# Kernel tuning notes

Hardware: AMD Instinct MI355X
Metric: run time of the kernel (lower is better)

The kernel has to match this reference:

```python
import jax, jax.numpy as jnp
import numpy as np

NHEAD, DK, DV = 8, 32, 32
GRAPH = [[1,2,3,6,7],[1,2,4],[1,3,5],[2,4],[3,5],[1,6,8,12],[1,7,9,13],[6,8,10],[7,9,13],[8,10],[9,11],[9,12,14],[11,13,15],[12,14,16],[13,15,17],[14,16],[15,17]]
_idx = np.zeros((17,5), np.int32); _val = np.zeros((17,5), bool)
for _i, _nb in enumerate(GRAPH):
    for _j, _n in enumerate(_nb):
        _idx[_i,_j] = _n-1; _val[_i,_j] = True
NBR_IDX = jnp.asarray(_idx)            # (17,5) neighbor table (pad idx 0)
NBR_VALID = jnp.asarray(_val)          # (17,5) valid-neighbor mask
ATT_MASK = jnp.asarray(np.concatenate([_val, np.ones((17,2), bool)], 1))  # (17,7): 5 local + 2 global keys
INV_SQRT_DK = float(1.0/np.sqrt(DK))

def _ln_c(x, g, b, eps=1e-6):
    # LayerNorm over channel axis of (B,C,L)
    m = x.mean(1, keepdims=True)
    v = x.var(1, keepdims=True)
    return (x - m) * jax.lax.rsqrt(v + eps) * g[None,:,None] + b[None,:,None]

def _bn3(x, g, b, eps=1e-5):
    # BatchNorm1d (training batch stats) per channel over (B,L); x:(B,C,L)
    m = x.mean((0,2), keepdims=True)
    v = x.var((0,2), keepdims=True)
    return (x - m) * jax.lax.rsqrt(v + eps) * g[None,:,None] + b[None,:,None]

def _pos_ffn(x, w1, b1, w2, b2, g, b):
    # x:(B,C,L); Linear over C, relu, Linear back, residual, BatchNorm1d
    h = jax.nn.relu(jnp.einsum('bcl,hc->bhl', x, w1) + b1[None,:,None])
    y = jnp.einsum('bhl,ch->bcl', h, w2) + b2[None,:,None] + x
    return _bn3(y, g, b)

def _unfold(t):
    # t:(B,C,17) -> (B,C,5,17): per-node 5-wide neighbor window, zero padded
    g = t[:,:,NBR_IDX]                              # (B,C,17,5)
    g = jnp.where(NBR_VALID[None,None], g, 0.0)
    return jnp.transpose(g, (0,1,3,2))

def _sju(xn, ax, wq,bq,wk,bk,wv,bv, bng,bnb, f1w,f1b,f2w,f2b,fg,fb):
    B, C, L = xn.shape
    q = (jnp.einsum('oc,bcl->bol', wq, xn) + bq[None,:,None]).reshape(B,NHEAD,DK,L)
    kx = jnp.einsum('oc,bcl->bol', wk, xn) + bk[None,:,None]
    vx = jnp.einsum('oc,bcl->bol', wv, xn) + bv[None,:,None]
    k = _unfold(kx).reshape(B,NHEAD,DK,5,L)
    v = _unfold(vx).reshape(B,NHEAD,DV,5,L)
    ak = (jnp.einsum('oc,bcal->boal', wk, ax) + bk[None,:,None,None]).reshape(B,NHEAD,DK,2,L)
    av = (jnp.einsum('oc,bcal->boal', wv, ax) + bv[None,:,None,None]).reshape(B,NHEAD,DV,2,L)
    k = jnp.concatenate([k, ak], 3)                 # (B,H,dk,7,L)
    v = jnp.concatenate([v, av], 3)
    pre = jnp.einsum('bhdl,bhdwl->bhwl', q, k) * INV_SQRT_DK
    pre = jnp.where(ATT_MASK.T[None,None], pre, -jnp.inf)
    a = jax.nn.softmax(pre, axis=2)
    att = jnp.einsum('bhwl,bhdwl->bhdl', a, v).reshape(B,C,L)
    ret = _bn3(xn + att, bng, bnb)
    return _pos_ffn(ret, f1w,f1b,f2w,f2b,fg,fb)

def _sru(x, y, wq,bq,wk,bk,wv,bv, bng,bnb, f1w,f1b,f2w,f2b,fg,fb):
    # x:(B,C) relay, y:(B,C,Ly) keys/values
    B, C = x.shape
    q = (x @ wq.T + bq).reshape(B,NHEAD,DK)
    k = (jnp.einsum('oc,bcl->bol', wk, y) + bk[None,:,None]).reshape(B,NHEAD,DK,-1)
    v = (jnp.einsum('oc,bcl->bol', wv, y) + bv[None,:,None]).reshape(B,NHEAD,DV,-1)
    a = jax.nn.softmax(jnp.einsum('bhd,bhdl->bhl', q, k) * INV_SQRT_DK, axis=2)
    att = jnp.einsum('bhl,bhdl->bhd', a, v).reshape(B,C)
    ret = _bn3((x + att)[:,:,None], bng, bnb)
    return _pos_ffn(ret, f1w,f1b,f2w,f2b,fg,fb)[:,:,0]

def _forward(data, ln_g, ln_b, jq_w, jq_b, jk_w, jk_b, jv_w, jv_b, jbn_g, jbn_b, jf1_w, jf1_b, jf2_w, jf2_b, jfbn_g, jfbn_b, rq_w, rq_b, rk_w, rk_b, rv_w, rv_b, rbn_g, rbn_b, rf1_w, rf1_b, rf2_w, rf2_b, rfbn_g, rfbn_b):
    B, C, V, T = data.shape
    embs = jnp.transpose(data, (0,3,1,2)).reshape(B*T, C, V)   # fold time into batch
    nodes = embs
    relay = embs.mean(2)                                       # (BT,C)
    # ax: per node the 2 extra keys = its own original embedding + relay (fixed across layers)
    ax = jnp.stack([embs, jnp.broadcast_to(relay[:,:,None], embs.shape)], axis=2)  # (BT,C,2,V)
    for i in range(ln_g.shape[0]):
        xn = _ln_c(nodes, ln_g[i], ln_b[i])
        nodes = jax.nn.leaky_relu(_sju(xn, ax, jq_w[i],jq_b[i],jk_w[i],jk_b[i],jv_w[i],jv_b[i],jbn_g[i],jbn_b[i],jf1_w[i],jf1_b[i],jf2_w[i],jf2_b[i],jfbn_g[i],jfbn_b[i]), 0.01)
        y = jnp.concatenate([relay[:,:,None], nodes], axis=2)   # (BT,C,18)
        relay = jax.nn.leaky_relu(_sru(relay, y, rq_w[i],rq_b[i],rk_w[i],rk_b[i],rv_w[i],rv_b[i],rbn_g[i],rbn_b[i],rf1_w[i],rf1_b[i],rf2_w[i],rf2_b[i],rfbn_g[i],rfbn_b[i]), 0.01)
    return jnp.transpose(nodes.reshape(B,T,C,V), (0,2,3,1))

def setup_inputs():
    key = jax.random.key(0)
    Lyr, C, DIN, B, T, V = 2, 256, 1024, 4, 256, 17
    ks = jax.random.split(key, 40)
    ctr = [0]
    def nxt():
        k = ks[ctr[0]]; ctr[0] += 1; return k
    def w(shape, s=0.05):
        return jax.random.normal(nxt(), shape, jnp.float32) * s
    ones = lambda: jnp.ones((Lyr, C), jnp.float32)
    zeros = lambda: jnp.zeros((Lyr, C), jnp.float32)
    inp = {'data': jax.random.normal(nxt(), (B,C,V,T), jnp.float32),
           'ln_g': ones(), 'ln_b': zeros()}
    for p in ('j', 'r'):
        inp[p+'q_w'] = w((Lyr,C,C)); inp[p+'q_b'] = w((Lyr,C))
        inp[p+'k_w'] = w((Lyr,C,C)); inp[p+'k_b'] = w((Lyr,C))
        inp[p+'v_w'] = w((Lyr,C,C)); inp[p+'v_b'] = w((Lyr,C))
        inp[p+'bn_g'] = ones(); inp[p+'bn_b'] = zeros()
        inp[p+'f1_w'] = w((Lyr,DIN,C)); inp[p+'f1_b'] = w((Lyr,DIN))
        inp[p+'f2_w'] = w((Lyr,C,DIN)); inp[p+'f2_b'] = w((Lyr,C))
        inp[p+'fbn_g'] = ones(); inp[p+'fbn_b'] = zeros()
    return inp

def reference(data, ln_g, ln_b, jq_w, jq_b, jk_w, jk_b, jv_w, jv_b, jbn_g, jbn_b, jf1_w, jf1_b, jf2_w, jf2_b, jfbn_g, jfbn_b, rq_w, rq_b, rk_w, rk_b, rv_w, rv_b, rbn_g, rbn_b, rf1_w, rf1_b, rf2_w, rf2_b, rfbn_g, rfbn_b):
    return _forward(data, ln_g, ln_b, jq_w, jq_b, jk_w, jk_b, jv_w, jv_b, jbn_g, jbn_b, jf1_w, jf1_b, jf2_w, jf2_b, jfbn_g, jfbn_b, rq_w, rq_b, rk_w, rk_b, rv_w, rv_b, rbn_g, rbn_b, rf1_w, rf1_b, rf2_w, rf2_b, rfbn_g, rfbn_b)
```

## Files before the change

### kernel.cpp

```cpp
#include <hip/hip_runtime.h>
#include <hip/hip_bf16.h>


using bf16 = __hip_bfloat16;
typedef __attribute__((ext_vector_type(8))) short bf16x8v;
typedef __attribute__((ext_vector_type(4))) float f32x4;

namespace {
constexpr int kBT = 1024;
constexpr int kC = 256;
constexpr int kV = 17;
constexpr int kT = 256;
constexpr int kDIN = 1024;
constexpr int kRows = kBT * kV;
constexpr int kRowsE = kRows + kBT;
constexpr float kInvSqrtDk = 0.17677669529663687f;
constexpr size_t SZ_BIG = (size_t)kRows * kC;
}

__constant__ int c_nbi[17][5] = {
    {0, 1, 2, 5, 6},   {0, 1, 3, 0, 0},   {0, 2, 4, 0, 0},  {1, 3, 0, 0, 0},
    {2, 4, 0, 0, 0},   {0, 5, 7, 11, 0},  {0, 6, 8, 12, 0}, {5, 7, 9, 0, 0},
    {6, 8, 12, 0, 0},  {7, 9, 0, 0, 0},   {8, 10, 0, 0, 0}, {8, 11, 13, 0, 0},
    {10, 12, 14, 0, 0},{11, 13, 15, 0, 0},{12, 14, 16, 0, 0},
    {13, 15, 0, 0, 0}, {14, 16, 0, 0, 0}};
__constant__ int c_ncnt[17] = {5, 3, 3, 2, 2, 4, 4, 3, 3, 2, 2, 3, 3, 3, 3, 2, 2};

__device__ inline float bf2f(unsigned short s) {
  unsigned int u = ((unsigned int)s) << 16;
  float f;
  __builtin_memcpy(&f, &u, 4);
  return f;
}
__device__ inline unsigned short f2bf(float f) {
  unsigned int u;
  __builtin_memcpy(&u, &f, 4);
  unsigned int r = (u + 0x7fffu + ((u >> 16) & 1u)) >> 16;
  return (unsigned short)r;
}
__device__ inline float4 ldbf4(const bf16* p) {
  ushort4 u = *(const ushort4*)p;
  return make_float4(bf2f(u.x), bf2f(u.y), bf2f(u.z), bf2f(u.w));
}
__device__ inline void stbf4(bf16* p, float4 v) {
  ushort4 u = make_ushort4(f2bf(v.x), f2bf(v.y), f2bf(v.z), f2bf(v.w));
  *(ushort4*)p = u;
}
__device__ inline float dot4(float4 a, float4 b) {
  return a.x * b.x + a.y * b.y + a.z * b.z + a.w * b.w;
}

__device__ inline void async16(const bf16* g, bf16* l) {
  __builtin_amdgcn_global_load_lds(
      (const __attribute__((address_space(1))) void*)g,
      (__attribute__((address_space(3))) void*)l, 16, 0, 0);
}

template <int KT>
__global__ __launch_bounds__(256) void k_mfma_gemm(
    const bf16* __restrict__ A, const bf16* __restrict__ W,
    const float* __restrict__ bias, const float* __restrict__ res,
    float* __restrict__ outF, bf16* __restrict__ outB, int N, int flags) {
  __shared__ bf16 As[2][128 * 64];
  __shared__ bf16 Bs[2][128 * 64];
  const int tid = threadIdx.x;
  const int wave = tid >> 6;
  const int lane = tid & 63;
  const int row0 = blockIdx.x * 128;
  const int col0 = blockIdx.y * 128;

  const int sub = lane >> 2;
  const int kq = (lane & 3) * 8;
  const int rg0 = (2 * wave + 0) * 16;
  const int rg1 = (2 * wave + 1) * 16;
  const bf16* ag0 = A + (size_t)(row0 + rg0 + sub) * KT + kq;
  const bf16* ag1 = A + (size_t)(row0 + rg1 + sub) * KT + kq;
  const bf16* bg0 = W + (size_t)(col0 + rg0 + sub) * KT + kq;
  const bf16* bg1 = W + (size_t)(col0 + rg1 + sub) * KT + kq;

  const int wm = wave >> 1, wn = wave & 1;
  const int fr = lane & 15;
  const int fk = (lane >> 4) * 8;

  f32x4 acc[4][4];
#pragma unroll
  for (int i = 0; i < 4; ++i)
#pragma unroll
    for (int j = 0; j < 4; ++j) acc[i][j] = (f32x4){0.f, 0.f, 0.f, 0.f};

#define STAGE64(buf, koff)                                   \
  do {                                                       \
    _Pragma("unroll") for (int kc = 0; kc < 2; ++kc) {       \
      const int off = (koff) + kc * 32;                      \
      async16(ag0 + off, &As[(buf)][kc * 4096 + rg0 * 32]);  \
      async16(ag1 + off, &As[(buf)][kc * 4096 + rg1 * 32]);  \
      async16(bg0 + off, &Bs[(buf)][kc * 4096 + rg0 * 32]);  \
      async16(bg1 + off, &Bs[(buf)][kc * 4096 + rg1 * 32]);  \
    }                                                        \
  } while (0)

  STAGE64(0, 0);
  __syncthreads();

  for (int k0 = 0; k0 < KT; k0 += 64) {
    const int cur = (k0 >> 6) & 1;
    if (k0 + 64 < KT) STAGE64(cur ^ 1, k0 + 64);
#pragma unroll
    for (int kc = 0; kc < 2; ++kc) {
      bf16x8v af[4], bfv[4];
#pragma unroll
      for (int i = 0; i < 4; ++i)
        af[i] = *(const bf16x8v*)&As[cur][kc * 4096 +
                                          (wm * 64 + i * 16 + fr) * 32 + fk];
#pragma unroll
      for (int j = 0; j < 4; ++j)
        bfv[j] = *(const bf16x8v*)&Bs[cur][kc * 4096 +
                                           (wn * 64 + j * 16 + fr) * 32 + fk];
#pragma unroll
      for (int i = 0; i < 4; ++i)
#pragma unroll
        for (int j = 0; j < 4; ++j)
          acc[i][j] = __builtin_amdgcn_mfma_f32_16x16x32_bf16(af[i], bfv[j],
                                                              acc[i][j], 0, 0,
                                                              0);
    }
    __syncthreads();
  }
#undef STAGE64

  if (flags & 4) {
    unsigned short* cs = (unsigned short*)As;
#pragma unroll
    for (int j = 0; j < 4; ++j) {
      int lc = wn * 64 + j * 16 + fr;
      float bv = bias ? bias[col0 + lc] : 0.f;
#pragma unroll
      for (int i = 0; i < 4; ++i) {
        int lr = wm * 64 + i * 16 + (lane >> 4) * 4;
#pragma unroll
        for (int r = 0; r < 4; ++r) {
          float v = acc[i][j][r] + bv;
          if (flags & 1) v = fmaxf(v, 0.f);
          cs[(lr + r) * 128 + lc] = f2bf(v);
        }
      }
    }
    __syncthreads();
#pragma unroll
    for (int p = 0; p < 8; ++p) {
      int lr = p * 16 + (tid >> 4);
      int lc = (tid & 15) * 8;
      *(bf16x8v*)&outB[(size_t)(row0 + lr) * N + col0 + lc] =
          *(const bf16x8v*)&cs[lr * 128 + lc];
    }
  } else {
    const int crow = row0 + wm * 64;
    const int ccol = col0 + wn * 64;
#pragma unroll
    for (int j = 0; j < 4; ++j) {
      int col = ccol + j * 16 + fr;
      float bv = bias ? bias[col] : 0.f;
#pragma unroll
      for (int i = 0; i < 4; ++i) {
        int rowb = crow + i * 16 + (lane >> 4) * 4;
#pragma unroll
        for (int r = 0; r < 4; ++r) {
          size_t row = (size_t)(rowb + r);
          float v = acc[i][j][r] + bv;
          if (res) v += res[row * N + col];
          if (flags & 1) v = fmaxf(v, 0.f);
          outF[row * N + col] = v;
        }
      }
    }
  }
}

__global__ __launch_bounds__(256) void k_xform_in(const float* __restrict__ data,
                                                  float* __restrict__ nodes,
                                                  bf16* __restrict__ embs_bf) {
  __shared__ float tile[32][33];
  int ct = blockIdx.x * 32, tt = blockIdx.y * 32;
  int bv = blockIdx.z;
  int b = bv / kV, v = bv - b * kV;
  int tx = threadIdx.x & 31, ty = threadIdx.x >> 5;
  for (int i = ty; i < 32; i += 8)
    tile[i][tx] = data[(((size_t)b * kC + ct + i) * kV + v) * kT + tt + tx];
  __syncthreads();
  for (int i = ty; i < 32; i += 8) {
    size_t s = (size_t)b * kT + tt + i;
    size_t idx = (s * kV + v) * kC + ct + tx;
    float val = tile[tx][i];
    nodes[idx] = val;
    embs_bf[idx] = __float2bfloat16(val);
  }
}

__global__ __launch_bounds__(256) void k_xform_out(const float* __restrict__ nodes,
                                                   float* __restrict__ out) {
  __shared__ float tile[32][33];
  int ct = blockIdx.x * 32, tt = blockIdx.y * 32;
  int bv = blockIdx.z;
  int b = bv / kV, v = bv - b * kV;
  int tx = threadIdx.x & 31, ty = threadIdx.x >> 5;
  for (int i = ty; i < 32; i += 8) {
    size_t s = (size_t)b * kT + tt + i;
    tile[i][tx] = nodes[(s * kV + v) * kC + ct + tx];
  }
  __syncthreads();
  for (int i = ty; i < 32; i += 8)
    out[(((size_t)b * kC + ct + i) * kV + v) * kT + tt + tx] = tile[tx][i];
}

__global__ __launch_bounds__(256) void k_relay_init(const float* __restrict__ nodes,
                                                    bf16* __restrict__ relay0_bf) {
  int t = threadIdx.x;
  int s = blockIdx.x * 4 + (t >> 6);
  int c4 = (t & 63) * 4;
  float4 acc = make_float4(0.f, 0.f, 0.f, 0.f);
#pragma unroll
  for (int v = 0; v < kV; ++v) {
    float4 x = *(const float4*)(nodes + ((size_t)s * kV + v) * kC + c4);
    acc.x += x.x; acc.y += x.y; acc.z += x.z; acc.w += x.w;
  }
  float4 r = make_float4(acc.x / 17.f, acc.y / 17.f, acc.z / 17.f, acc.w / 17.f);
  stbf4(relay0_bf + (size_t)s * kC + c4, r);
}

__global__ __launch_bounds__(256) void k_layernorm(const float* __restrict__ X,
                                                   const float* __restrict__ g,
                                                   const float* __restrict__ b,
                                                   float* __restrict__ O,
                                                   bf16* __restrict__ Ob) {
  int t = threadIdx.x;
  int row = blockIdx.x * 4 + (t >> 6);
  int c4 = (t & 63) * 4;
  size_t i = (size_t)row * kC + c4;
  float4 x = *(const float4*)(X + i);
  float s = x.x + x.y + x.z + x.w;
  float q = dot4(x, x);
#pragma unroll
  for (int o = 32; o >= 1; o >>= 1) {
    s += __shfl_xor(s, o);
    q += __shfl_xor(q, o);
  }
  float m = s * (1.f / 256.f);
  float var = q * (1.f / 256.f) - m * m;
  float rs = rsqrtf(var + 1e-6f);
  float4 g4 = *(const float4*)(g + c4);
  float4 b4 = *(const float4*)(b + c4);
  float4 o4 = make_float4((x.x - m) * rs * g4.x + b4.x,
                          (x.y - m) * rs * g4.y + b4.y,
                          (x.z - m) * rs * g4.z + b4.z,
                          (x.w - m) * rs * g4.w + b4.w);
  *(float4*)(O + i) = o4;
  stbf4(Ob + i, o4);
}

__global__ __launch_bounds__(256) void k_attn_sat(const bf16* __restrict__ qkv,
                                                  const bf16* __restrict__ akav,
                                                  float* __restrict__ z) {
  int t = threadIdx.x;
  int rl = blockIdx.x * 4 + (t >> 6);
  int lane = t & 63;
  int s = rl / kV, l = rl - s * kV;
  int c4 = lane * 4;
  float4 q = ldbf4(qkv + (size_t)rl * 768 + c4);
  int cnt = c_ncnt[l];
  float sc[7];
  int nrow[5];
#pragma unroll
  for (int w = 0; w < 5; ++w) {
    nrow[w] = s * kV + c_nbi[l][w];
    float4 k = ldbf4(qkv + (size_t)nrow[w] * 768 + 256 + c4);
    float p = dot4(q, k);
    p += __shfl_xor(p, 1, 8);
    p += __shfl_xor(p, 2, 8);
    p += __shfl_xor(p, 4, 8);
    sc[w] = (w < cnt) ? p * kInvSqrtDk : -1e30f;
  }
  {
    float4 k = ldbf4(akav + (size_t)rl * 1024 + c4);
    float p = dot4(q, k);
    p += __shfl_xor(p, 1, 8);
    p += __shfl_xor(p, 2, 8);
    p += __shfl_xor(p, 4, 8);
    sc[5] = p * kInvSqrtDk;
  }
  {
    float4 k = ldbf4(akav + (size_t)(kRows + s) * 1024 + c4);
    float p = dot4(q, k);
    p += __shfl_xor(p, 1, 8);
    p += __shfl_xor(p, 2, 8);
    p += __shfl_xor(p, 4, 8);
    sc[6] = p * kInvSqrtDk;
  }
  float mx = sc[0];
#pragma unroll
  for (int w = 1; w < 7; ++w) mx = fmaxf(mx, sc[w]);
  float den = 0.f;
#pragma unroll
  for (int w = 0; w < 7; ++w) {
    sc[w] = __expf(sc[w] - mx);
    den += sc[w];
  }
  float inv = 1.f / den;
  float4 acc = make_float4(0.f, 0.f, 0.f, 0.f);
#pragma unroll
  for (int w = 0; w < 5; ++w) {
    float4 v = ldbf4(qkv + (size_t)nrow[w] * 768 + 512 + c4);
    acc.x += sc[w] * v.x; acc.y += sc[w] * v.y;
    acc.z += sc[w] * v.z; acc.w += sc[w] * v.w;
  }
  {
    float4 v = ldbf4(akav + (size_t)rl * 1024 + 256 + c4);
    acc.x += sc[5] * v.x; acc.y += sc[5] * v.y;
    acc.z += sc[5] * v.z; acc.w += sc[5] * v.w;
  }
  {
    float4 v = ldbf4(akav + (size_t)(kRows + s) * 1024 + 256 + c4);
    acc.x += sc[6] * v.x; acc.y += sc[6] * v.y;
    acc.z += sc[6] * v.z; acc.w += sc[6] * v.w;
  }
  size_t zi = (size_t)rl * kC + c4;
  float4 xv = *(const float4*)(z + zi);
  *(float4*)(z + zi) = make_float4(xv.x + acc.x * inv, xv.y + acc.y * inv,
                                   xv.z + acc.z * inv, xv.w + acc.w * inv);
}

__global__ __launch_bounds__(256) void k_bn_partial(const float* __restrict__ A,
                                                    float* __restrict__ part,
                                                    int nb) {
  int c = threadIdx.x, blk = blockIdx.x;
  int lo = blk * 16;
  float s = 0.f, q = 0.f;
#pragma unroll
  for (int r = 0; r < 16; ++r) {
    float v = A[(size_t)(lo + r) * kC + c];
    s += v;
    q += v * v;
  }
  part[(size_t)blk * kC + c] = s;
  part[(size_t)(nb + blk) * kC + c] = q;
}

__global__ __launch_bounds__(256) void k_bn_finalize(const float* __restrict__ part,
                                                     int nb, float inv_n,
                                                     const float* __restrict__ g,
                                                     const float* __restrict__ b,
                                                     float* __restrict__ scale,
                                                     float* __restrict__ shift) {
  int c = blockIdx.x;
  int t = threadIdx.x;
  float s = 0.f, q = 0.f;
  for (int i = t; i < nb; i += 256) {
    s += part[(size_t)i * kC + c];
    q += part[(size_t)(nb + i) * kC + c];
  }
#pragma unroll
  for (int o = 32; o >= 1; o >>= 1) {
    s += __shfl_xor(s, o);
    q += __shfl_xor(q, o);
  }
  __shared__ float ws[4], wq[4];
  int wid = t >> 6;
  if ((t & 63) == 0) { ws[wid] = s; wq[wid] = q; }
  __syncthreads();
  if (t == 0) {
    float S = ws[0] + ws[1] + ws[2] + ws[3];
    float Q = wq[0] + wq[1] + wq[2] + wq[3];
    float m = S * inv_n;
    float var = Q * inv_n - m * m;
    float sc = g[c] * rsqrtf(var + 1e-5f);
    scale[c] = sc;
    shift[c] = b[c] - m * sc;
  }
}

__global__ __launch_bounds__(256) void k_bn_apply(const float* __restrict__ Z,
                                                  const float* __restrict__ scale,
                                                  const float* __restrict__ shift,
                                                  float* __restrict__ outF,
                                                  bf16* __restrict__ outB,
                                                  int leaky) {
  int t = threadIdx.x;
  int row = blockIdx.x * 4 + (t >> 6);
  int c4 = (t & 63) * 4;
  size_t i = (size_t)row * kC + c4;
  float4 z = *(const float4*)(Z + i);
  float4 sc = *(const float4*)(scale + c4);
  float4 sh = *(const float4*)(shift + c4);
  float4 v = make_float4(z.x * sc.x + sh.x, z.y * sc.y + sh.y,
                         z.z * sc.z + sh.z, z.w * sc.w + sh.w);
  if (leaky) {
    v.x = (v.x > 0.f) ? v.x : 0.01f * v.x;
    v.y = (v.y > 0.f) ? v.y : 0.01f * v.y;
    v.z = (v.z > 0.f) ? v.z : 0.01f * v.z;
    v.w = (v.w > 0.f) ? v.w : 0.01f * v.w;
  }
  if (outF) *(float4*)(outF + i) = v;
  if (outB) stbf4(outB + i, v);
}

__global__ __launch_bounds__(256) void k_bn_ln(
    const float* __restrict__ Z, const float* __restrict__ scale,
    const float* __restrict__ shift, const float* __restrict__ g,
    const float* __restrict__ b, float* __restrict__ nodesOut,
    float* __restrict__ xnOut, bf16* __restrict__ actOut) {
  int t = threadIdx.x;
  int row = blockIdx.x * 4 + (t >> 6);
  int c4 = (t & 63) * 4;
  size_t i = (size_t)row * kC + c4;
  float4 z = *(const float4*)(Z + i);
  float4 sc = *(const float4*)(scale + c4);
  float4 sh = *(const float4*)(shift + c4);
  float4 v = make_float4(z.x * sc.x + sh.x, z.y * sc.y + sh.y,
                         z.z * sc.z + sh.z, z.w * sc.w + sh.w);
  v.x = (v.x > 0.f) ? v.x : 0.01f * v.x;
  v.y = (v.y > 0.f) ? v.y : 0.01f * v.y;
  v.z = (v.z > 0.f) ? v.z : 0.01f * v.z;
  v.w = (v.w > 0.f) ? v.w : 0.01f * v.w;
  *(float4*)(nodesOut + i) = v;
  float s = v.x + v.y + v.z + v.w;
  float q = dot4(v, v);
#pragma unroll
  for (int o = 32; o >= 1; o >>= 1) {
    s += __shfl_xor(s, o);
    q += __shfl_xor(q, o);
  }
  float m = s * (1.f / 256.f);
  float var = q * (1.f / 256.f) - m * m;
  float rs = rsqrtf(var + 1e-6f);
  float4 g4 = *(const float4*)(g + c4);
  float4 b4 = *(const float4*)(b + c4);
  float4 o4 = make_float4((v.x - m) * rs * g4.x + b4.x,
                          (v.y - m) * rs * g4.y + b4.y,
                          (v.z - m) * rs * g4.z + b4.z,
                          (v.w - m) * rs * g4.w + b4.w);
  *(float4*)(xnOut + i) = o4;
  stbf4(actOut + i, o4);
}

struct CvtTab {
  const float* src[12];
  bf16* dst[12];
  int n[12];
};
__global__ __launch_bounds__(256) void k_cvt_multi(CvtTab t) {
  int c = blockIdx.y;
  int i = (blockIdx.x * 256 + threadIdx.x) * 4;
  if (i >= t.n[c]) return;
  float4 v = *(const float4*)(t.src[c] + i);
  stbf4(t.dst[c] + i, v);
}

struct BiasTab {
  const float* src[10];
  float* dst[10];
};
__global__ __launch_bounds__(256) void k_bias_cat(BiasTab t) {
  t.dst[blockIdx.x][threadIdx.x] = t.src[blockIdx.x][threadIdx.x];
}

extern "C" void kernel_launch(void* const* d_in, const int* in_sizes, int n_in,
                              void* d_out, int out_size, void* d_ws, size_t ws_size,
                              hipStream_t stream) {
  const float* data = (const float*)d_in[0];
  const float* ln_g = (const float*)d_in[1];
  const float* ln_b = (const float*)d_in[2];
  const float* jq_w = (const float*)d_in[3];
  const float* jq_b = (const float*)d_in[4];
  const float* jk_w = (const float*)d_in[5];
  const float* jk_b = (const float*)d_in[6];
  const float* jv_w = (const float*)d_in[7];
  const float* jv_b = (const float*)d_in[8];
  const float* jbn_g = (const float*)d_in[9];
  const float* jbn_b = (const float*)d_in[10];
  const float* jf1_w = (const float*)d_in[11];
  const float* jf1_b = (const float*)d_in[12];
  const float* jf2_w = (const float*)d_in[13];
  const float* jf2_b = (const float*)d_in[14];
  const float* jfbn_g = (const float*)d_in[15];
  const float* jfbn_b = (const float*)d_in[16];
  float* out = (float*)d_out;

  float* f = (float*)d_ws;
  float* nodes = f;    f += SZ_BIG;
  float* xn = f;       f += SZ_BIG;
  float* part = f;     f += 2 * 1088 * kC;
  float* scale = f;    f += kC;
  float* shift = f;    f += kC;
  float* cb_jqkv = f;  f += 2 * 768;
  float* cb_kv4 = f;   f += 1024;

  bf16* bfa = (bf16*)f;
  bf16* act_bf = bfa;   bfa += SZ_BIG;
  bf16* embsX_bf = bfa; bfa += (size_t)kRowsE * kC;
  bf16* P = bfa;        bfa += (size_t)kRows * kDIN;
  bf16* akavBuf = bfa;  bfa += (size_t)kRowsE * 1024;
  bf16* Wjqkv = bfa;    bfa += 2 * 768 * 256;
  bf16* Wkv4 = bfa;     bfa += 1024 * 256;
  bf16* Wjf1 = bfa;     bfa += 2 * 1024 * 256;
  bf16* Wjf2 = bfa;     bfa += 2 * 256 * 1024;

  bf16* relay0_bf = embsX_bf + SZ_BIG;
  bf16* qkv_bf = P;
  bf16* h_bf = P;
  float* y2 = xn;

  auto gemm = [&](const bf16* A, const bf16* W, const float* bias,
                  const float* res, float* oF, bf16* oB, int M, int N, int K,
                  int flags) {
    dim3 g(M / 128, N / 128);
    if (K == 256)
      k_mfma_gemm<256><<<g, 256, 0, stream>>>(A, W, bias, res, oF, oB, N,
                                              flags);
    else
      k_mfma_gemm<1024><<<g, 256, 0, stream>>>(A, W, bias, res, oF, oB, N,
                                               flags);
  };

  {
    CvtTab t;
    for (int i = 0; i < 2; ++i) {
      const size_t om = (size_t)i * kC * kC;
      const float* s3[3] = {jq_w + om, jk_w + om, jv_w + om};
      bf16* d3[3] = {Wjqkv + (size_t)i * 768 * 256,
                     Wjqkv + (size_t)i * 768 * 256 + 65536,
                     Wjqkv + (size_t)i * 768 * 256 + 131072};
      for (int j = 0; j < 3; ++j) {
        t.src[i * 3 + j] = s3[j];
        t.dst[i * 3 + j] = d3[j];
        t.n[i * 3 + j] = 65536;
      }
    }
    t.src[6] = jk_w;                 t.dst[6] = Wkv4;               t.n[6] = 65536;
    t.src[7] = jv_w;                 t.dst[7] = Wkv4 + 65536;       t.n[7] = 65536;
    t.src[8] = jk_w + (size_t)65536; t.dst[8] = Wkv4 + 131072;      t.n[8] = 65536;
    t.src[9] = jv_w + (size_t)65536; t.dst[9] = Wkv4 + 196608;      t.n[9] = 65536;
    t.src[10] = jf1_w; t.dst[10] = Wjf1; t.n[10] = 2 * 1024 * 256;
    t.src[11] = jf2_w; t.dst[11] = Wjf2; t.n[11] = 2 * 256 * 1024;
    k_cvt_multi<<<dim3(512, 12), 256, 0, stream>>>(t);
  }
  {
    BiasTab t;
    for (int i = 0; i < 2; ++i) {
      t.src[i * 3 + 0] = jq_b + (size_t)i * kC;
      t.src[i * 3 + 1] = jk_b + (size_t)i * kC;
      t.src[i * 3 + 2] = jv_b + (size_t)i * kC;
      t.dst[i * 3 + 0] = cb_jqkv + i * 768;
      t.dst[i * 3 + 1] = cb_jqkv + i * 768 + 256;
      t.dst[i * 3 + 2] = cb_jqkv + i * 768 + 512;
    }
    t.src[6] = jk_b;       t.dst[6] = cb_kv4;
    t.src[7] = jv_b;       t.dst[7] = cb_kv4 + 256;
    t.src[8] = jk_b + kC;  t.dst[8] = cb_kv4 + 512;
    t.src[9] = jv_b + kC;  t.dst[9] = cb_kv4 + 768;
    k_bias_cat<<<10, 256, 0, stream>>>(t);
  }

  k_xform_in<<<dim3(8, 8, 4 * kV), 256, 0, stream>>>(data, nodes, embsX_bf);
  k_relay_init<<<kBT / 4, 256, 0, stream>>>(nodes, relay0_bf);

  gemm(embsX_bf, Wkv4, cb_kv4, nullptr, nullptr, akavBuf, kRowsE, 1024, 256, 4);

  k_layernorm<<<kRows / 4, 256, 0, stream>>>(nodes, ln_g, ln_b, xn, act_bf);

  for (int i = 0; i < 2; ++i) {
    const size_t ob = (size_t)i * kC, ofb1 = (size_t)i * kDIN;
    const bf16* Wj = Wjqkv + (size_t)i * 768 * 256;
    const bf16* Wf1 = Wjf1 + (size_t)i * 1024 * 256;
    const bf16* Wf2 = Wjf2 + (size_t)i * 256 * 1024;
    const float* cbj = cb_jqkv + i * 768;
    const int nb = kRows / 16;

    gemm(act_bf, Wj, cbj, nullptr, nullptr, qkv_bf, kRows, 768, 256, 4);
    k_attn_sat<<<kRows / 4, 256, 0, stream>>>(qkv_bf, akavBuf + (size_t)i * 512,
                                              xn);
    k_bn_partial<<<nb, 256, 0, stream>>>(xn, part, nb);
    k_bn_finalize<<<kC, 256, 0, stream>>>(part, nb, 1.f / kRows, jbn_g + ob,
                                          jbn_b + ob, scale, shift);
    k_bn_apply<<<kRows / 4, 256, 0, stream>>>(xn, scale, shift, nodes, act_bf,
                                              0);
    gemm(act_bf, Wf1, jf1_b + ofb1, nullptr, nullptr, h_bf, kRows, 1024, 256,
         4 | 1);
    gemm(h_bf, Wf2, jf2_b + ob, nodes, y2, nullptr, kRows, 256, 1024, 2);
    k_bn_partial<<<nb, 256, 0, stream>>>(y2, part, nb);
    k_bn_finalize<<<kC, 256, 0, stream>>>(part, nb, 1.f / kRows, jfbn_g + ob,
                                          jfbn_b + ob, scale, shift);
    if (i == 0) {
      k_bn_ln<<<kRows / 4, 256, 0, stream>>>(y2, scale, shift, ln_g + kC,
                                             ln_b + kC, nodes, xn, act_bf);
    } else {
      k_bn_apply<<<kRows / 4, 256, 0, stream>>>(y2, scale, shift, nodes,
                                                nullptr, 1);
    }
  }

  k_xform_out<<<dim3(8, 8, 4 * kV), 256, 0, stream>>>(nodes, out);
  (void)in_sizes; (void)n_in; (void)out_size; (void)ws_size;
}
```

Baseline: 441.8 us.

## Fuse BatchNorm statistics and apply into attention, GEMM epilogue and output transpose

Per-channel BatchNorm partial sums are now computed inside the attention kernel and in the FFN2 GEMM epilogue, which removes the separate k_bn_partial passes. The FFN residual applies the first BN's scale and shift on the fly, and the final BN plus leaky ReLU is folded into the output transpose. This drops redundant writes of the nodes buffer and several kernel launches. In exchange the finalize step has to reduce many more partial rows (one per 4-row attention block), and the GEMM epilogue gains shuffles, a shared-memory reduction and an extra barrier.

New measurement: 431.7 us. 2.3% less time.

```diff
diff --git a/kernel.cpp b/kernel.cpp
--- a/kernel.cpp
+++ b/kernel.cpp
@@ -60,7 +60,9 @@
 __global__ __launch_bounds__(256) void k_mfma_gemm(
     const bf16* __restrict__ A, const bf16* __restrict__ W,
     const float* __restrict__ bias, const float* __restrict__ res,
-    float* __restrict__ outF, bf16* __restrict__ outB, int N, int flags) {
+    float* __restrict__ outF, bf16* __restrict__ outB,
+    const float* __restrict__ bnScI, const float* __restrict__ bnShI,
+    float* __restrict__ partOut, int nbPart, int N, int flags) {
   __shared__ bf16 As[2][128 * 64];
   __shared__ bf16 Bs[2][128 * 64];
   const int tid = threadIdx.x;
@@ -156,10 +158,14 @@
   } else {
     const int crow = row0 + wm * 64;
     const int ccol = col0 + wn * 64;
+    float colS[4] = {0.f, 0.f, 0.f, 0.f};
+    float colQ[4] = {0.f, 0.f, 0.f, 0.f};
 #pragma unroll
     for (int j = 0; j < 4; ++j) {
       int col = ccol + j * 16 + fr;
       float bv = bias ? bias[col] : 0.f;
+      float rsc = 1.f, rsh = 0.f;
+      if (flags & 8) { rsc = bnScI[col]; rsh = bnShI[col]; }
 #pragma unroll
       for (int i = 0; i < 4; ++i) {
         int rowb = crow + i * 16 + (lane >> 4) * 4;
@@ -167,10 +173,39 @@
         for (int r = 0; r < 4; ++r) {
           size_t row = (size_t)(rowb + r);
           float v = acc[i][j][r] + bv;
-          if (res) v += res[row * N + col];
+          if (res) v += res[row * N + col] * rsc + rsh;
           if (flags & 1) v = fmaxf(v, 0.f);
           outF[row * N + col] = v;
+          colS[j] += v;
+          colQ[j] += v * v;
         }
+      }
+    }
+    if (flags & 8) {
+#pragma unroll
+      for (int j = 0; j < 4; ++j) {
+        colS[j] += __shfl_xor(colS[j], 16);
+        colS[j] += __shfl_xor(colS[j], 32);
+        colQ[j] += __shfl_xor(colQ[j], 16);
+        colQ[j] += __shfl_xor(colQ[j], 32);
+      }
+      float* sred = (float*)As;
+      float* qred = sred + 4 * 64;
+      if (lane < 16) {
+#pragma unroll
+        for (int j = 0; j < 4; ++j) {
+          sred[wave * 64 + j * 16 + fr] = colS[j];
+          qred[wave * 64 + j * 16 + fr] = colQ[j];
+        }
+      }
+      __syncthreads();
+      if (tid < 128) {
+        int wn2 = tid >> 6, c = tid & 63;
+        float s = sred[wn2 * 64 + c] + sred[(wn2 | 2) * 64 + c];
+        float q = qred[wn2 * 64 + c] + qred[(wn2 | 2) * 64 + c];
+        int col = col0 + wn2 * 64 + c;
+        partOut[(size_t)blockIdx.x * kC + col] = s;
+        partOut[(size_t)(nbPart + blockIdx.x) * kC + col] = q;
       }
     }
   }
@@ -196,16 +231,21 @@
   }
 }
 
-__global__ __launch_bounds__(256) void k_xform_out(const float* __restrict__ nodes,
+__global__ __launch_bounds__(256) void k_xform_out(const float* __restrict__ Z,
+                                                   const float* __restrict__ scale,
+                                                   const float* __restrict__ shift,
                                                    float* __restrict__ out) {
   __shared__ float tile[32][33];
   int ct = blockIdx.x * 32, tt = blockIdx.y * 32;
   int bv = blockIdx.z;
   int b = bv / kV, v = bv - b * kV;
   int tx = threadIdx.x & 31, ty = threadIdx.x >> 5;
+  float sc = scale[ct + tx], sh = shift[ct + tx];
   for (int i = ty; i < 32; i += 8) {
     size_t s = (size_t)b * kT + tt + i;
-    tile[i][tx] = nodes[(s * kV + v) * kC + ct + tx];
+    float val = Z[(s * kV + v) * kC + ct + tx] * sc + sh;
+    val = (val > 0.f) ? val : 0.01f * val;
+    tile[i][tx] = val;
   }
   __syncthreads();
   for (int i = ty; i < 32; i += 8)
@@ -259,9 +299,14 @@
 
 __global__ __launch_bounds__(256) void k_attn_sat(const bf16* __restrict__ qkv,
                                                   const bf16* __restrict__ akav,
-                                                  float* __restrict__ z) {
+                                                  float* __restrict__ z,
+                                                  float* __restrict__ part,
+                                                  int nb) {
+  __shared__ float sS[4][256];
+  __shared__ float qS[4][256];
   int t = threadIdx.x;
-  int rl = blockIdx.x * 4 + (t >> 6);
+  int w = t >> 6;
+  int rl = blockIdx.x * 4 + w;
   int lane = t & 63;
   int s = rl / kV, l = rl - s * kV;
   int c4 = lane * 4;
@@ -270,14 +315,14 @@
   float sc[7];
   int nrow[5];
 #pragma unroll
-  for (int w = 0; w < 5; ++w) {
-    nrow[w] = s * kV + c_nbi[l][w];
-    float4 k = ldbf4(qkv + (size_t)nrow[w] * 768 + 256 + c4);
+  for (int wd = 0; wd < 5; ++wd) {
+    nrow[wd] = s * kV + c_nbi[l][wd];
+    float4 k = ldbf4(qkv + (size_t)nrow[wd] * 768 + 256 + c4);
     float p = dot4(q, k);
     p += __shfl_xor(p, 1, 8);
     p += __shfl_xor(p, 2, 8);
     p += __shfl_xor(p, 4, 8);
-    sc[w] = (w < cnt) ? p * kInvSqrtDk : -1e30f;
+    sc[wd] = (wd < cnt) ? p * kInvSqrtDk : -1e30f;
   }
   {
     float4 k = ldbf4(akav + (size_t)rl * 1024 + c4);
@@ -297,20 +342,20 @@
   }
   float mx = sc[0];
 #pragma unroll
-  for (int w = 1; w < 7; ++w) mx = fmaxf(mx, sc[w]);
+  for (int wd = 1; wd < 7; ++wd) mx = fmaxf(mx, sc[wd]);
   float den = 0.f;
 #pragma unroll
-  for (int w = 0; w < 7; ++w) {
-    sc[w] = __expf(sc[w] - mx);
-    den += sc[w];
+  for (int wd = 0; wd < 7; ++wd) {
+    sc[wd] = __expf(sc[wd] - mx);
+    den += sc[wd];
   }
   float inv = 1.f / den;
   float4 acc = make_float4(0.f, 0.f, 0.f, 0.f);
 #pragma unroll
-  for (int w = 0; w < 5; ++w) {
-    float4 v = ldbf4(qkv + (size_t)nrow[w] * 768 + 512 + c4);
-    acc.x += sc[w] * v.x; acc.y += sc[w] * v.y;
-    acc.z += sc[w] * v.z; acc.w += sc[w] * v.w;
+  for (int wd = 0; wd < 5; ++wd) {
+    float4 v = ldbf4(qkv + (size_t)nrow[wd] * 768 + 512 + c4);
+    acc.x += sc[wd] * v.x; acc.y += sc[wd] * v.y;
+    acc.z += sc[wd] * v.z; acc.w += sc[wd] * v.w;
   }
   {
     float4 v = ldbf4(akav + (size_t)rl * 1024 + 256 + c4);
@@ -324,24 +369,18 @@
   }
   size_t zi = (size_t)rl * kC + c4;
   float4 xv = *(const float4*)(z + zi);
-  *(float4*)(z + zi) = make_float4(xv.x + acc.x * inv, xv.y + acc.y * inv,
-                                   xv.z + acc.z * inv, xv.w + acc.w * inv);
-}
-
-__global__ __launch_bounds__(256) void k_bn_partial(const float* __restrict__ A,
-                                                    float* __restrict__ part,
-                                                    int nb) {
-  int c = threadIdx.x, blk = blockIdx.x;
-  int lo = blk * 16;
-  float s = 0.f, q = 0.f;
-#pragma unroll
-  for (int r = 0; r < 16; ++r) {
-    float v = A[(size_t)(lo + r) * kC + c];
-    s += v;
-    q += v * v;
-  }
-  part[(size_t)blk * kC + c] = s;
-  part[(size_t)(nb + blk) * kC + c] = q;
+  float4 o = make_float4(xv.x + acc.x * inv, xv.y + acc.y * inv,
+                         xv.z + acc.z * inv, xv.w + acc.w * inv);
+  *(float4*)(z + zi) = o;
+  sS[w][c4 + 0] = o.x; sS[w][c4 + 1] = o.y;
+  sS[w][c4 + 2] = o.z; sS[w][c4 + 3] = o.w;
+  qS[w][c4 + 0] = o.x * o.x; qS[w][c4 + 1] = o.y * o.y;
+  qS[w][c4 + 2] = o.z * o.z; qS[w][c4 + 3] = o.w * o.w;
+  __syncthreads();
+  float ps = sS[0][t] + sS[1][t] + sS[2][t] + sS[3][t];
+  float pq = qS[0][t] + qS[1][t] + qS[2][t] + qS[3][t];
+  part[(size_t)blockIdx.x * kC + t] = ps;
+  part[(size_t)(nb + blockIdx.x) * kC + t] = pq;
 }
 
 __global__ __launch_bounds__(256) void k_bn_finalize(const float* __restrict__ part,
@@ -405,8 +444,8 @@
 __global__ __launch_bounds__(256) void k_bn_ln(
     const float* __restrict__ Z, const float* __restrict__ scale,
     const float* __restrict__ shift, const float* __restrict__ g,
-    const float* __restrict__ b, float* __restrict__ nodesOut,
-    float* __restrict__ xnOut, bf16* __restrict__ actOut) {
+    const float* __restrict__ b, float* __restrict__ xnOut,
+    bf16* __restrict__ actOut) {
   int t = threadIdx.x;
   int row = blockIdx.x * 4 + (t >> 6);
   int c4 = (t & 63) * 4;
@@ -420,7 +459,6 @@
   v.y = (v.y > 0.f) ? v.y : 0.01f * v.y;
   v.z = (v.z > 0.f) ? v.z : 0.01f * v.z;
   v.w = (v.w > 0.f) ? v.w : 0.01f * v.w;
-  *(float4*)(nodesOut + i) = v;
   float s = v.x + v.y + v.z + v.w;
   float q = dot4(v, v);
 #pragma unroll
@@ -487,7 +525,7 @@
   float* f = (float*)d_ws;
   float* nodes = f;    f += SZ_BIG;
   float* xn = f;       f += SZ_BIG;
-  float* part = f;     f += 2 * 1088 * kC;
+  float* part = f;     f += 2 * (kRows / 4) * kC;
   float* scale = f;    f += kC;
   float* shift = f;    f += kC;
   float* cb_jqkv = f;  f += 2 * 768;
@@ -509,14 +547,16 @@
   float* y2 = xn;
 
   auto gemm = [&](const bf16* A, const bf16* W, const float* bias,
-                  const float* res, float* oF, bf16* oB, int M, int N, int K,
-                  int flags) {
+                  const float* res, float* oF, bf16* oB, const float* bnScI,
+                  const float* bnShI, float* partOut, int nbPart, int M, int N,
+                  int K, int flags) {
     dim3 g(M / 128, N / 128);
     if (K == 256)
-      k_mfma_gemm<256><<<g, 256, 0, stream>>>(A, W, bias, res, oF, oB, N,
-                                              flags);
+      k_mfma_gemm<256><<<g, 256, 0, stream>>>(A, W, bias, res, oF, oB, bnScI,
+                                              bnShI, partOut, nbPart, N, flags);
     else
-      k_mfma_gemm<1024><<<g, 256, 0, stream>>>(A, W, bias, res, oF, oB, N,
+      k_mfma_gemm<1024><<<g, 256, 0, stream>>>(A, W, bias, res, oF, oB, bnScI,
+                                               bnShI, partOut, nbPart, N,
                                                flags);
   };
 
@@ -562,7 +602,8 @@
   k_xform_in<<<dim3(8, 8, 4 * kV), 256, 0, stream>>>(data, nodes, embsX_bf);
   k_relay_init<<<kBT / 4, 256, 0, stream>>>(nodes, relay0_bf);
 
-  gemm(embsX_bf, Wkv4, cb_kv4, nullptr, nullptr, akavBuf, kRowsE, 1024, 256, 4);
+  gemm(embsX_bf, Wkv4, cb_kv4, nullptr, nullptr, akavBuf, nullptr, nullptr,
+       nullptr, 0, kRowsE, 1024, 256, 4);
 
   k_layernorm<<<kRows / 4, 256, 0, stream>>>(nodes, ln_g, ln_b, xn, act_bf);
 
@@ -572,31 +613,29 @@
     const bf16* Wf1 = Wjf1 + (size_t)i * 1024 * 256;
     const bf16* Wf2 = Wjf2 + (size_t)i * 256 * 1024;
     const float* cbj = cb_jqkv + i * 768;
-    const int nb = kRows / 16;
-
-    gemm(act_bf, Wj, cbj, nullptr, nullptr, qkv_bf, kRows, 768, 256, 4);
+    const int nbA = kRows / 4;
+    const int nbG = kRows / 128;
+
+    gemm(act_bf, Wj, cbj, nullptr, nullptr, qkv_bf, nullptr, nullptr, nullptr,
+         0, kRows, 768, 256, 4);
     k_attn_sat<<<kRows / 4, 256, 0, stream>>>(qkv_bf, akavBuf + (size_t)i * 512,
-                                              xn);
-    k_bn_partial<<<nb, 256, 0, stream>>>(xn, part, nb);
-    k_bn_finalize<<<kC, 256, 0, stream>>>(part, nb, 1.f / kRows, jbn_g + ob,
+                                              xn, part, nbA);
+    k_bn_finalize<<<kC, 256, 0, stream>>>(part, nbA, 1.f / kRows, jbn_g + ob,
                                           jbn_b + ob, scale, shift);
-    k_bn_apply<<<kRows / 4, 256, 0, stream>>>(xn, scale, shift, nodes, act_bf,
-                                              0);
-    gemm(act_bf, Wf1, jf1_b + ofb1, nullptr, nullptr, h_bf, kRows, 1024, 256,
-         4 | 1);
-    gemm(h_bf, Wf2, jf2_b + ob, nodes, y2, nullptr, kRows, 256, 1024, 2);
-    k_bn_partial<<<nb, 256, 0, stream>>>(y2, part, nb);
-    k_bn_finalize<<<kC, 256, 0, stream>>>(part, nb, 1.f / kRows, jfbn_g + ob,
+    k_bn_apply<<<kRows / 4, 256, 0, stream>>>(xn, scale, shift, nullptr,
+                                              act_bf, 0);
+    gemm(act_bf, Wf1, jf1_b + ofb1, nullptr, nullptr, h_bf, nullptr, nullptr,
+         nullptr, 0, kRows, 1024, 256, 4 | 1);
+    gemm(h_bf, Wf2, jf2_b + ob, xn, y2, nullptr, scale, shift, part, nbG,
+         kRows, 256, 1024, 2 | 8);
+    k_bn_finalize<<<kC, 256, 0, stream>>>(part, nbG, 1.f / kRows, jfbn_g + ob,
                                           jfbn_b + ob, scale, shift);
     if (i == 0) {
       k_bn_ln<<<kRows / 4, 256, 0, stream>>>(y2, scale, shift, ln_g + kC,
-                                             ln_b + kC, nodes, xn, act_bf);
-    } else {
-      k_bn_apply<<<kRows / 4, 256, 0, stream>>>(y2, scale, shift, nodes,
-                                                nullptr, 1);
-    }
-  }
-
-  k_xform_out<<<dim3(8, 8, 4 * kV), 256, 0, stream>>>(nodes, out);
+                                             ln_b + kC, xn, act_bf);
+    }
+  }
+
+  k_xform_out<<<dim3(8, 8, 4 * kV), 256, 0, stream>>>(y2, scale, shift, out);
   (void)in_sizes; (void)n_in; (void)out_size; (void)ws_size;
 }
```
